# Kernel optimization log

Measured on AMD Instinct MI355X. Metric: run time of the kernel, lower is better.

## Reference

```python
import jax, jax.numpy as jnp
import numpy as np

HEADS, OUT_CH = 8, 32  # GATConv(128, 256//8, heads=8) -> concat width 256
NEG_SLOPE = 0.2


def setup_inputs() -> dict:
    key = jax.random.key(0)
    ks = jax.random.split(key, 12)
    N, E, F_IN = 50000, 500000, 128
    H, C = HEADS, OUT_CH
    HID = H * C            # 256
    x = jax.random.normal(ks[0], (N, F_IN), dtype=jnp.float32)
    edge_index = jax.random.randint(ks[1], (2, E), 0, N, dtype=jnp.int64)
    s = 1.0 / np.sqrt(F_IN)
    W_gat = jax.random.normal(ks[2], (F_IN, H * C), dtype=jnp.float32) * s
    att_src = jax.random.normal(ks[3], (H, C), dtype=jnp.float32) * (1.0 / np.sqrt(C))
    att_dst = jax.random.normal(ks[4], (H, C), dtype=jnp.float32) * (1.0 / np.sqrt(C))
    b_gat = jnp.zeros((HID,), dtype=jnp.float32)
    W1 = jax.random.normal(ks[5], (HID, HID // 2), dtype=jnp.float32) * (1.0 / np.sqrt(HID))
    b1 = jnp.zeros((HID // 2,), dtype=jnp.float32)
    W2 = jax.random.normal(ks[6], (HID // 2, 6), dtype=jnp.float32) * (1.0 / np.sqrt(HID // 2))
    b2 = jnp.zeros((6,), dtype=jnp.float32)
    return {"x": x, "edge_index": edge_index, "W_gat": W_gat, "att_src": att_src,
            "att_dst": att_dst, "b_gat": b_gat, "W1": W1, "b1": b1, "W2": W2, "b2": b2}


def _gat_forward(x, edge_index, W_gat, att_src, att_dst, b_gat):
    N = x.shape[0]
    H, C = HEADS, OUT_CH
    # add self loops (PyG GATConv default)
    loop = jnp.arange(N, dtype=edge_index.dtype)
    src = jnp.concatenate([edge_index[0], loop])
    dst = jnp.concatenate([edge_index[1], loop])
    # per-node transform: [N, H, C]
    xh = (x @ W_gat).reshape(N, H, C)
    a_src = jnp.einsum('nhc,hc->nh', xh, att_src)  # [N, H]
    a_dst = jnp.einsum('nhc,hc->nh', xh, att_dst)  # [N, H]
    alpha = a_src[src] + a_dst[dst]                # [Etot, H]
    alpha = jnp.where(alpha >= 0, alpha, NEG_SLOPE * alpha)  # leaky relu
    # segment softmax over destination nodes
    m = jax.ops.segment_max(alpha, dst, num_segments=N)     # [N, H]
    m = jax.lax.stop_gradient(m)
    ex = jnp.exp(alpha - m[dst])
    denom = jax.ops.segment_sum(ex, dst, num_segments=N)    # [N, H]
    coef = ex / denom[dst]                                   # [Etot, H]
    # weighted scatter-add aggregation
    msgs = xh[src] * coef[:, :, None]                        # [Etot, H, C]
    out = jax.ops.segment_sum(msgs, dst, num_segments=N)     # [N, H, C]
    return out.reshape(N, H * C) + b_gat


def reference(x, edge_index, W_gat, att_src, att_dst, b_gat, W1, b1, W2, b2):
    h = _gat_forward(x, edge_index, W_gat, att_src, att_dst, b_gat)
    h = jax.nn.elu(h)
    g = jnp.mean(h, axis=0, keepdims=True)   # [1, 256] mean pool
    g = jax.nn.relu(g @ W1 + b1)
    return g @ W2 + b2                        # [1, 6] logits
```

## Files before the change

kernel.cpp:

```cpp
#include <hip/hip_runtime.h>
#include <hip/hip_fp8.h>
#include <math.h>

#define F_IN 128
#define HID 256
#define NH 8
#define CAP 40

typedef _Float16 h16;
typedef __attribute__((ext_vector_type(8))) _Float16 half8;
typedef __attribute__((ext_vector_type(4))) float f32x4;

__device__ inline unsigned char f32_to_fp8(float v) {
#if __has_builtin(__builtin_amdgcn_cvt_pk_fp8_f32)
    return (unsigned char)(__builtin_amdgcn_cvt_pk_fp8_f32(v, v, 0, false) & 0xff);
#else
    __hip_fp8_e4m3 t(v);
    return (unsigned char)t.__x;
#endif
}

__device__ inline void fp8x4_to_f32(int w, float* out) {
#if __has_builtin(__builtin_amdgcn_cvt_pk_f32_fp8)
    auto lo = __builtin_amdgcn_cvt_pk_f32_fp8(w, false);
    auto hi = __builtin_amdgcn_cvt_pk_f32_fp8(w, true);
    out[0] = lo[0]; out[1] = lo[1]; out[2] = hi[0]; out[3] = hi[1];
#else
    #pragma unroll
    for (int k = 0; k < 4; ++k) {
        __hip_fp8_e4m3 t;
        t.__x = (unsigned char)((w >> (8 * k)) & 0xff);
        out[k] = (float)t;
    }
#endif
}

__global__ void k_prep(const float* __restrict__ Wg, h16* __restrict__ Wt_sw,
                       int* cnt, float* g2, int n) {
    int i = blockIdx.x * 256 + threadIdx.x;
    if (i < n) cnt[i] = 0;
    if (i < 256 * HID) g2[i] = 0.f;
    if (i < 4096) {
        int fid = i;
        int lane16 = fid & 15;
        int quad = (fid >> 4) & 3;
        int ks = (fid >> 6) & 3;
        int ct = fid >> 8;
        int col = ct * 16 + lane16;
        int k0 = ks * 32 + quad * 8;
        half8 v;
        #pragma unroll
        for (int j = 0; j < 8; ++j) v[j] = (h16)Wg[(size_t)(k0 + j) * HID + col];
        *(half8*)(Wt_sw + (size_t)fid * 8) = v;
    }
}

__global__ __launch_bounds__(512) void k_gemmsc(const float* __restrict__ x,
                                                const h16* __restrict__ Wt_sw,
                                                const float* __restrict__ att_s,
                                                const float* __restrict__ att_d,
                                                const int* __restrict__ srcp,
                                                const int* __restrict__ dstp,
                                                unsigned char* __restrict__ xh8,
                                                float* __restrict__ a_src,
                                                float* __restrict__ a_dst,
                                                int* cnt, unsigned short* __restrict__ bin,
                                                int n, int e, int ntiles) {
    __shared__ h16 wlds[32768];
    int t = threadIdx.x;
    {
        const int4* wsrc = (const int4*)Wt_sw;
        int4* wdst = (int4*)wlds;
        #pragma unroll
        for (int i = 0; i < 8; ++i) wdst[i * 512 + t] = wsrc[i * 512 + t];
    }
    __syncthreads();
    int w = t >> 6, l = t & 63;
    int lane16 = l & 15, quad = l >> 4;
    const h16* wl = wlds + (size_t)l * 8;

    if (w >= 6) {
        for (int i = blockIdx.x * 128 + (w - 6) * 64 + l; i < e; i += gridDim.x * 128) {
            int d = dstp[i];
            int pos = atomicAdd(&cnt[d], 1);
            if (pos < CAP) bin[(size_t)d * CAP + pos] = (unsigned short)srcp[i];
        }
        return;
    }
    for (int tile = blockIdx.x * 6 + w; tile < ntiles; tile += gridDim.x * 6) {
        int row0 = tile * 16;
        int rA = row0 + lane16;
        if (rA >= n) rA = n - 1;
        const float* xrow = x + (size_t)rA * F_IN + quad * 8;
        half8 afr[4];
        #pragma unroll
        for (int ks = 0; ks < 4; ++ks) {
            float4 v0 = *(const float4*)(xrow + ks * 32);
            float4 v1 = *(const float4*)(xrow + ks * 32 + 4);
            half8 a;
            a[0] = (h16)v0.x; a[1] = (h16)v0.y; a[2] = (h16)v0.z; a[3] = (h16)v0.w;
            a[4] = (h16)v1.x; a[5] = (h16)v1.y; a[6] = (h16)v1.z; a[7] = (h16)v1.w;
            afr[ks] = a;
        }
        f32x4 acc[16];
        #pragma unroll
        for (int ct = 0; ct < 16; ++ct) acc[ct] = (f32x4){0.f, 0.f, 0.f, 0.f};
        #pragma unroll
        for (int ct = 0; ct < 16; ++ct) {
            #pragma unroll
            for (int ks = 0; ks < 4; ++ks) {
                half8 b = *(const half8*)(wl + (ct * 4 + ks) * 512);
                acc[ct] = __builtin_amdgcn_mfma_f32_16x16x32_f16(afr[ks], b, acc[ct], 0, 0, 0);
            }
        }
        if (row0 + 16 <= n) {
            #pragma unroll
            for (int ct = 0; ct < 16; ++ct) {
                int col = ct * 16 + lane16;
                #pragma unroll
                for (int r = 0; r < 4; ++r)
                    xh8[(size_t)(row0 + quad * 4 + r) * HID + col] = f32_to_fp8(acc[ct][r]);
            }
        } else {
            #pragma unroll
            for (int ct = 0; ct < 16; ++ct) {
                int col = ct * 16 + lane16;
                #pragma unroll
                for (int r = 0; r < 4; ++r) {
                    int row = row0 + quad * 4 + r;
                    if (row < n) xh8[(size_t)row * HID + col] = f32_to_fp8(acc[ct][r]);
                }
            }
        }
        #pragma unroll
        for (int h = 0; h < 8; ++h) {
            float ps[4] = {0.f, 0.f, 0.f, 0.f};
            float pd[4] = {0.f, 0.f, 0.f, 0.f};
            #pragma unroll
            for (int cc = 0; cc < 2; ++cc) {
                int ct = h * 2 + cc;
                float as_ = att_s[ct * 16 + lane16];
                float ad_ = att_d[ct * 16 + lane16];
                #pragma unroll
                for (int r = 0; r < 4; ++r) {
                    ps[r] += acc[ct][r] * as_;
                    pd[r] += acc[ct][r] * ad_;
                }
            }
            #pragma unroll
            for (int m = 1; m < 16; m <<= 1) {
                #pragma unroll
                for (int r = 0; r < 4; ++r) {
                    ps[r] += __shfl_xor(ps[r], m, 64);
                    pd[r] += __shfl_xor(pd[r], m, 64);
                }
            }
            if (lane16 == 0) {
                #pragma unroll
                for (int r = 0; r < 4; ++r) {
                    int row = row0 + quad * 4 + r;
                    if (row < n) {
                        a_src[row * NH + h] = ps[r];
                        a_dst[row * NH + h] = pd[r];
                    }
                }
            }
        }
    }
}

__global__ __launch_bounds__(256) void k_agg(const unsigned char* __restrict__ xh8,
                                             const float* __restrict__ a_src,
                                             const float* __restrict__ a_dst,
                                             const int* __restrict__ cnt,
                                             const unsigned short* __restrict__ bin,
                                             const float* __restrict__ b_gat,
                                             float* __restrict__ g2, int n) {
    __shared__ float wpart[4][260];
    int t = threadIdx.x;
    int slot = t >> 4;
    int cl = t & 15;
    int c0 = cl * 16;
    int h = cl >> 1;
    int nn = blockIdx.x * 16 + slot;
    bool alive = nn < n;
    int nnc = alive ? nn : (n - 1);

    float ad = a_dst[nnc * NH + h];
    int deg = cnt[nnc];
    if (deg > CAP) deg = CAP;

    float al = a_src[nnc * NH + h] + ad;
    al = al > 0.f ? al : 0.2f * al;
    float ex = __expf(al);
    float den = ex;
    float acc[16];
    {
        int4 v = *(const int4*)(xh8 + (size_t)nnc * HID + c0);
        float f[16];
        fp8x4_to_f32(v.x, f); fp8x4_to_f32(v.y, f + 4);
        fp8x4_to_f32(v.z, f + 8); fp8x4_to_f32(v.w, f + 12);
        #pragma unroll
        for (int i = 0; i < 16; ++i) acc[i] = ex * f[i];
    }
    const unsigned short* brow = bin + (size_t)nnc * CAP;
    int j = 0;
    for (; j + 4 <= deg; j += 4) {
        ushort4 ss = *(const ushort4*)(brow + j);
        int s0 = ss.x, s1 = ss.y, s2 = ss.z, s3 = ss.w;
        float aa[4];
        aa[0] = a_src[s0 * NH + h];
        aa[1] = a_src[s1 * NH + h];
        aa[2] = a_src[s2 * NH + h];
        aa[3] = a_src[s3 * NH + h];
        int4 v0 = *(const int4*)(xh8 + (size_t)s0 * HID + c0);
        int4 v1 = *(const int4*)(xh8 + (size_t)s1 * HID + c0);
        int4 v2 = *(const int4*)(xh8 + (size_t)s2 * HID + c0);
        int4 v3 = *(const int4*)(xh8 + (size_t)s3 * HID + c0);
        float e4[4];
        #pragma unroll
        for (int q = 0; q < 4; ++q) {
            float a2 = aa[q] + ad;
            a2 = a2 > 0.f ? a2 : 0.2f * a2;
            e4[q] = __expf(a2);
            den += e4[q];
        }
        float f[16];
        fp8x4_to_f32(v0.x, f); fp8x4_to_f32(v0.y, f + 4);
        fp8x4_to_f32(v0.z, f + 8); fp8x4_to_f32(v0.w, f + 12);
        #pragma unroll
        for (int i = 0; i < 16; ++i) acc[i] += e4[0] * f[i];
        fp8x4_to_f32(v1.x, f); fp8x4_to_f32(v1.y, f + 4);
        fp8x4_to_f32(v1.z, f + 8); fp8x4_to_f32(v1.w, f + 12);
        #pragma unroll
        for (int i = 0; i < 16; ++i) acc[i] += e4[1] * f[i];
        fp8x4_to_f32(v2.x, f); fp8x4_to_f32(v2.y, f + 4);
        fp8x4_to_f32(v2.z, f + 8); fp8x4_to_f32(v2.w, f + 12);
        #pragma unroll
        for (int i = 0; i < 16; ++i) acc[i] += e4[2] * f[i];
        fp8x4_to_f32(v3.x, f); fp8x4_to_f32(v3.y, f + 4);
        fp8x4_to_f32(v3.z, f + 8); fp8x4_to_f32(v3.w, f + 12);
        #pragma unroll
        for (int i = 0; i < 16; ++i) acc[i] += e4[3] * f[i];
    }
    for (; j < deg; ++j) {
        int s = brow[j];
        float a2 = a_src[s * NH + h] + ad;
        a2 = a2 > 0.f ? a2 : 0.2f * a2;
        float e2 = __expf(a2);
        den += e2;
        int4 v = *(const int4*)(xh8 + (size_t)s * HID + c0);
        float f[16];
        fp8x4_to_f32(v.x, f); fp8x4_to_f32(v.y, f + 4);
        fp8x4_to_f32(v.z, f + 8); fp8x4_to_f32(v.w, f + 12);
        #pragma unroll
        for (int i = 0; i < 16; ++i) acc[i] += e2 * f[i];
    }
    float inv = 1.f / den;
    float val[16];
    #pragma unroll
    for (int q = 0; q < 4; ++q) {
        float4 bv = *(const float4*)(b_gat + c0 + q * 4);
        val[q * 4 + 0] = acc[q * 4 + 0] * inv + bv.x;
        val[q * 4 + 1] = acc[q * 4 + 1] * inv + bv.y;
        val[q * 4 + 2] = acc[q * 4 + 2] * inv + bv.z;
        val[q * 4 + 3] = acc[q * 4 + 3] * inv + bv.w;
    }
    #pragma unroll
    for (int i = 0; i < 16; ++i) {
        float v = val[i];
        v = v > 0.f ? v : expm1f(v);
        val[i] = alive ? v : 0.f;
    }
    #pragma unroll
    for (int i = 0; i < 16; ++i) {
        val[i] += __shfl_xor(val[i], 16, 64);
        val[i] += __shfl_xor(val[i], 32, 64);
    }
    int w = t >> 6, lw = t & 63;
    if (lw < 16) {
        #pragma unroll
        for (int q = 0; q < 4; ++q)
            *(f32x4*)(&wpart[w][c0 + q * 4]) =
                (f32x4){val[q * 4], val[q * 4 + 1], val[q * 4 + 2], val[q * 4 + 3]};
    }
    __syncthreads();
    float s = wpart[0][t] + wpart[1][t] + wpart[2][t] + wpart[3][t];
    atomicAdd(&g2[(blockIdx.x & 255) * HID + t], s);
}

__global__ __launch_bounds__(256) void k_mlp(const float* __restrict__ g2,
                                             const float* __restrict__ W1,
                                             const float* __restrict__ b1,
                                             const float* __restrict__ W2,
                                             const float* __restrict__ b2,
                                             float* __restrict__ out, int n) {
    __shared__ float gm[HID];
    __shared__ float h1p[2][128];
    __shared__ float h1[128];
    int t = threadIdx.x;
    float s = 0.f;
    for (int b = 0; b < 256; ++b) s += g2[b * HID + t];
    gm[t] = s / (float)n;
    __syncthreads();
    int o = t & 127, hf = t >> 7;
    float a = 0.f;
    #pragma unroll 4
    for (int k = hf * 128; k < hf * 128 + 128; ++k) a += gm[k] * W1[k * 128 + o];
    h1p[hf][o] = a;
    __syncthreads();
    if (t < 128) {
        float v = h1p[0][t] + h1p[1][t] + b1[t];
        h1[t] = v > 0.f ? v : 0.f;
    }
    __syncthreads();
    if (t < 6) {
        float a2 = b2[t];
        for (int k = 0; k < 128; ++k) a2 += h1[k] * W2[k * 6 + t];
        out[t] = a2;
    }
}

extern "C" void kernel_launch(void* const* d_in, const int* in_sizes, int n_in,
                              void* d_out, int out_size, void* d_ws, size_t ws_size,
                              hipStream_t stream) {
    const float* x     = (const float*)d_in[0];
    const int*   ei    = (const int*)d_in[1];
    const float* Wg    = (const float*)d_in[2];
    const float* att_s = (const float*)d_in[3];
    const float* att_d = (const float*)d_in[4];
    const float* b_gat = (const float*)d_in[5];
    const float* W1    = (const float*)d_in[6];
    const float* b1    = (const float*)d_in[7];
    const float* W2    = (const float*)d_in[8];
    const float* b2    = (const float*)d_in[9];

    int N = in_sizes[0] / F_IN;
    int E = in_sizes[1] / 2;
    const int* srcp = ei;
    const int* dstp = ei + E;
    int nblk = (N + 15) / 16;
    int ntiles = (N + 15) / 16;

    char* ws = (char*)d_ws;
    size_t off = 0;
    auto alloc = [&](size_t bytes) {
        size_t o = off;
        off += (bytes + 255) & ~(size_t)255;
        return o;
    };
    unsigned char* xh8 = (unsigned char*)(ws + alloc((size_t)N * HID));
    h16*   Wt      = (h16*)(ws + alloc((size_t)F_IN * HID * 2));
    float* asr     = (float*)(ws + alloc((size_t)N * NH * 4));
    float* ads     = (float*)(ws + alloc((size_t)N * NH * 4));
    int*   cnt     = (int*)(ws + alloc((size_t)N * 4));
    unsigned short* bin = (unsigned short*)(ws + alloc((size_t)N * CAP * 2));
    float* g2      = (float*)(ws + alloc((size_t)256 * HID * 4));

    k_prep<<<(N + 255) / 256, 256, 0, stream>>>(Wg, Wt, cnt, g2, N);
    k_gemmsc<<<512, 512, 0, stream>>>(x, Wt, att_s, att_d, srcp, dstp,
                                      xh8, asr, ads, cnt, bin, N, E, ntiles);
    k_agg<<<nblk, 256, 0, stream>>>(xh8, asr, ads, cnt, bin, b_gat, g2, N);
    k_mlp<<<1, 256, 0, stream>>>(g2, W1, b1, W2, b2, (float*)d_out, N);
}
```

Baseline: 176.7 us.

## Replace global atomic binning with two-pass bucketed partition and separate GEMM kernel

Edge binning by destination moves out of the GEMM kernel into two new kernels. The first partitions edges into 256-node buckets using shared-memory histograms and one global atomic per bucket per block. The second builds the per-node CAP-limited lists in LDS and writes them out with coalesced stores. This removes the per-edge global atomics and scattered 2-byte writes. The GEMM kernel now runs one tile per wave and issues its x loads before the weight LDS fill so they overlap, at the cost of two extra launches and a bucket buffer that drops edges past BCAP.

```diff
diff --git a/kernel.cpp b/kernel.cpp
--- a/kernel.cpp
+++ b/kernel.cpp
@@ -6,6 +6,7 @@
 #define HID 256
 #define NH 8
 #define CAP 40
+#define BCAP 4096
 
 typedef _Float16 h16;
 typedef __attribute__((ext_vector_type(8))) _Float16 half8;
@@ -36,9 +37,9 @@
 }
 
 __global__ void k_prep(const float* __restrict__ Wg, h16* __restrict__ Wt_sw,
-                       int* cnt, float* g2, int n) {
+                       int* gcur, float* g2, int n) {
     int i = blockIdx.x * 256 + threadIdx.x;
-    if (i < n) cnt[i] = 0;
+    if (i < 256) gcur[i] = 0;
     if (i < 256 * HID) g2[i] = 0.f;
     if (i < 4096) {
         int fid = i;
@@ -55,19 +56,105 @@
     }
 }
 
-__global__ __launch_bounds__(512) void k_gemmsc(const float* __restrict__ x,
-                                                const h16* __restrict__ Wt_sw,
-                                                const float* __restrict__ att_s,
-                                                const float* __restrict__ att_d,
-                                                const int* __restrict__ srcp,
-                                                const int* __restrict__ dstp,
-                                                unsigned char* __restrict__ xh8,
-                                                float* __restrict__ a_src,
-                                                float* __restrict__ a_dst,
-                                                int* cnt, unsigned short* __restrict__ bin,
-                                                int n, int e, int ntiles) {
+__global__ __launch_bounds__(256) void k_part(const int* __restrict__ dstp,
+                                              const int* __restrict__ srcp,
+                                              unsigned int* __restrict__ gbuck,
+                                              int* __restrict__ gcur,
+                                              int e, int nbuck) {
+    __shared__ int hist[256];
+    __shared__ int base[256];
+    __shared__ int cur[256];
+    int t = threadIdx.x;
+    int c0 = blockIdx.x * 4096;
+    hist[t] = 0;
+    __syncthreads();
+    #pragma unroll
+    for (int j = 0; j < 16; ++j) {
+        int i = c0 + j * 256 + t;
+        if (i < e) atomicAdd(&hist[dstp[i] >> 8], 1);
+    }
+    __syncthreads();
+    if (t < nbuck && hist[t] > 0) base[t] = atomicAdd(&gcur[t], hist[t]);
+    cur[t] = 0;
+    __syncthreads();
+    #pragma unroll
+    for (int j = 0; j < 16; ++j) {
+        int i = c0 + j * 256 + t;
+        if (i < e) {
+            int d = dstp[i];
+            int b = d >> 8;
+            int pos = base[b] + atomicAdd(&cur[b], 1);
+            if (pos < BCAP)
+                gbuck[(size_t)b * BCAP + pos] =
+                    ((unsigned)(d & 255) << 16) | (unsigned)srcp[i];
+        }
+    }
+}
+
+__global__ __launch_bounds__(256) void k_bin(const unsigned int* __restrict__ gbuck,
+                                             const int* __restrict__ gcur,
+                                             int* __restrict__ cnt,
+                                             unsigned short* __restrict__ bin,
+                                             int n, int nbuck) {
+    __shared__ int hist[256];
+    __shared__ int cur[256];
+    __shared__ __align__(16) unsigned short bl[256 * CAP];
+    int t = threadIdx.x;
+    int b = blockIdx.x;
+    int count = gcur[b];
+    if (count > BCAP) count = BCAP;
+    hist[t] = 0;
+    __syncthreads();
+    const unsigned int* bb = gbuck + (size_t)b * BCAP;
+    for (int j = t; j < count; j += 256) atomicAdd(&hist[(bb[j] >> 16) & 255], 1);
+    __syncthreads();
+    int node = b * 256 + t;
+    if (node < n) {
+        int hh = hist[t];
+        cnt[node] = hh > CAP ? CAP : hh;
+    }
+    cur[t] = 0;
+    __syncthreads();
+    for (int j = t; j < count; j += 256) {
+        unsigned int wv = bb[j];
+        int dl = (wv >> 16) & 255;
+        int pos = atomicAdd(&cur[dl], 1);
+        if (pos < CAP) bl[dl * CAP + pos] = (unsigned short)(wv & 0xffff);
+    }
+    __syncthreads();
+    const int4* s4 = (const int4*)bl;
+    int4* d4 = (int4*)(bin + (size_t)b * 256 * CAP);
+    #pragma unroll
+    for (int q = 0; q < 5; ++q) d4[q * 256 + t] = s4[q * 256 + t];
+}
+
+__global__ __launch_bounds__(512) void k_gemm(const float* __restrict__ x,
+                                              const h16* __restrict__ Wt_sw,
+                                              const float* __restrict__ att_s,
+                                              const float* __restrict__ att_d,
+                                              unsigned char* __restrict__ xh8,
+                                              float* __restrict__ a_src,
+                                              float* __restrict__ a_dst,
+                                              int n, int ntiles) {
     __shared__ h16 wlds[32768];
     int t = threadIdx.x;
+    int w = t >> 6, l = t & 63;
+    int lane16 = l & 15, quad = l >> 4;
+
+    float4 pv0[4], pv1[4];
+    int tile = blockIdx.x * 8 + w;
+    bool have = tile < ntiles;
+    int row0 = tile * 16;
+    if (have) {
+        int rA = row0 + lane16;
+        if (rA >= n) rA = n - 1;
+        const float* xrow = x + (size_t)rA * F_IN + quad * 8;
+        #pragma unroll
+        for (int ks = 0; ks < 4; ++ks) {
+            pv0[ks] = *(const float4*)(xrow + ks * 32);
+            pv1[ks] = *(const float4*)(xrow + ks * 32 + 4);
+        }
+    }
     {
         const int4* wsrc = (const int4*)Wt_sw;
         int4* wdst = (int4*)wlds;
@@ -75,94 +162,79 @@
         for (int i = 0; i < 8; ++i) wdst[i * 512 + t] = wsrc[i * 512 + t];
     }
     __syncthreads();
-    int w = t >> 6, l = t & 63;
-    int lane16 = l & 15, quad = l >> 4;
+    if (!have) return;
     const h16* wl = wlds + (size_t)l * 8;
 
-    if (w >= 6) {
-        for (int i = blockIdx.x * 128 + (w - 6) * 64 + l; i < e; i += gridDim.x * 128) {
-            int d = dstp[i];
-            int pos = atomicAdd(&cnt[d], 1);
-            if (pos < CAP) bin[(size_t)d * CAP + pos] = (unsigned short)srcp[i];
-        }
-        return;
-    }
-    for (int tile = blockIdx.x * 6 + w; tile < ntiles; tile += gridDim.x * 6) {
-        int row0 = tile * 16;
-        int rA = row0 + lane16;
-        if (rA >= n) rA = n - 1;
-        const float* xrow = x + (size_t)rA * F_IN + quad * 8;
-        half8 afr[4];
+    half8 afr[4];
+    #pragma unroll
+    for (int ks = 0; ks < 4; ++ks) {
+        half8 a;
+        a[0] = (h16)pv0[ks].x; a[1] = (h16)pv0[ks].y;
+        a[2] = (h16)pv0[ks].z; a[3] = (h16)pv0[ks].w;
+        a[4] = (h16)pv1[ks].x; a[5] = (h16)pv1[ks].y;
+        a[6] = (h16)pv1[ks].z; a[7] = (h16)pv1[ks].w;
+        afr[ks] = a;
+    }
+    f32x4 acc[16];
+    #pragma unroll
+    for (int ct = 0; ct < 16; ++ct) acc[ct] = (f32x4){0.f, 0.f, 0.f, 0.f};
+    #pragma unroll
+    for (int ct = 0; ct < 16; ++ct) {
         #pragma unroll
         for (int ks = 0; ks < 4; ++ks) {
-            float4 v0 = *(const float4*)(xrow + ks * 32);
-            float4 v1 = *(const float4*)(xrow + ks * 32 + 4);
-            half8 a;
-            a[0] = (h16)v0.x; a[1] = (h16)v0.y; a[2] = (h16)v0.z; a[3] = (h16)v0.w;
-            a[4] = (h16)v1.x; a[5] = (h16)v1.y; a[6] = (h16)v1.z; a[7] = (h16)v1.w;
-            afr[ks] = a;
-        }
-        f32x4 acc[16];
-        #pragma unroll
-        for (int ct = 0; ct < 16; ++ct) acc[ct] = (f32x4){0.f, 0.f, 0.f, 0.f};
+            half8 bfr = *(const half8*)(wl + (ct * 4 + ks) * 512);
+            acc[ct] = __builtin_amdgcn_mfma_f32_16x16x32_f16(afr[ks], bfr, acc[ct], 0, 0, 0);
+        }
+    }
+    if (row0 + 16 <= n) {
         #pragma unroll
         for (int ct = 0; ct < 16; ++ct) {
+            int col = ct * 16 + lane16;
             #pragma unroll
-            for (int ks = 0; ks < 4; ++ks) {
-                half8 b = *(const half8*)(wl + (ct * 4 + ks) * 512);
-                acc[ct] = __builtin_amdgcn_mfma_f32_16x16x32_f16(afr[ks], b, acc[ct], 0, 0, 0);
+            for (int r = 0; r < 4; ++r)
+                xh8[(size_t)(row0 + quad * 4 + r) * HID + col] = f32_to_fp8(acc[ct][r]);
+        }
+    } else {
+        #pragma unroll
+        for (int ct = 0; ct < 16; ++ct) {
+            int col = ct * 16 + lane16;
+            #pragma unroll
+            for (int r = 0; r < 4; ++r) {
+                int row = row0 + quad * 4 + r;
+                if (row < n) xh8[(size_t)row * HID + col] = f32_to_fp8(acc[ct][r]);
             }
         }
-        if (row0 + 16 <= n) {
+    }
+    #pragma unroll
+    for (int h = 0; h < 8; ++h) {
+        float ps[4] = {0.f, 0.f, 0.f, 0.f};
+        float pd[4] = {0.f, 0.f, 0.f, 0.f};
+        #pragma unroll
+        for (int cc = 0; cc < 2; ++cc) {
+            int ct = h * 2 + cc;
+            float as_ = att_s[ct * 16 + lane16];
+            float ad_ = att_d[ct * 16 + lane16];
             #pragma unroll
-            for (int ct = 0; ct < 16; ++ct) {
-                int col = ct * 16 + lane16;
-                #pragma unroll
-                for (int r = 0; r < 4; ++r)
-                    xh8[(size_t)(row0 + quad * 4 + r) * HID + col] = f32_to_fp8(acc[ct][r]);
+            for (int r = 0; r < 4; ++r) {
+                ps[r] += acc[ct][r] * as_;
+                pd[r] += acc[ct][r] * ad_;
             }
-        } else {
+        }
+        #pragma unroll
+        for (int m = 1; m < 16; m <<= 1) {
             #pragma unroll
-            for (int ct = 0; ct < 16; ++ct) {
-                int col = ct * 16 + lane16;
-                #pragma unroll
-                for (int r = 0; r < 4; ++r) {
-                    int row = row0 + quad * 4 + r;
-                    if (row < n) xh8[(size_t)row * HID + col] = f32_to_fp8(acc[ct][r]);
-                }
+            for (int r = 0; r < 4; ++r) {
+                ps[r] += __shfl_xor(ps[r], m, 64);
+                pd[r] += __shfl_xor(pd[r], m, 64);
             }
         }
-        #pragma unroll
-        for (int h = 0; h < 8; ++h) {
-            float ps[4] = {0.f, 0.f, 0.f, 0.f};
-            float pd[4] = {0.f, 0.f, 0.f, 0.f};
+        if (lane16 == 0) {
             #pragma unroll
-            for (int cc = 0; cc < 2; ++cc) {
-                int ct = h * 2 + cc;
-                float as_ = att_s[ct * 16 + lane16];
-                float ad_ = att_d[ct * 16 + lane16];
-                #pragma unroll
-                for (int r = 0; r < 4; ++r) {
-                    ps[r] += acc[ct][r] * as_;
-                    pd[r] += acc[ct][r] * ad_;
-                }
-            }
-            #pragma unroll
-            for (int m = 1; m < 16; m <<= 1) {
-                #pragma unroll
-                for (int r = 0; r < 4; ++r) {
-                    ps[r] += __shfl_xor(ps[r], m, 64);
-                    pd[r] += __shfl_xor(pd[r], m, 64);
-                }
-            }
-            if (lane16 == 0) {
-                #pragma unroll
-                for (int r = 0; r < 4; ++r) {
-                    int row = row0 + quad * 4 + r;
-                    if (row < n) {
-                        a_src[row * NH + h] = ps[r];
-                        a_dst[row * NH + h] = pd[r];
-                    }
+            for (int r = 0; r < 4; ++r) {
+                int row = row0 + quad * 4 + r;
+                if (row < n) {
+                    a_src[row * NH + h] = ps[r];
+                    a_dst[row * NH + h] = pd[r];
                 }
             }
         }
@@ -341,6 +413,7 @@
     const int* dstp = ei + E;
     int nblk = (N + 15) / 16;
     int ntiles = (N + 15) / 16;
+    int nbuck = (N + 255) >> 8;
 
     char* ws = (char*)d_ws;
     size_t off = 0;
@@ -354,12 +427,18 @@
     float* asr     = (float*)(ws + alloc((size_t)N * NH * 4));
     float* ads     = (float*)(ws + alloc((size_t)N * NH * 4));
     int*   cnt     = (int*)(ws + alloc((size_t)N * 4));
-    unsigned short* bin = (unsigned short*)(ws + alloc((size_t)N * CAP * 2));
+    unsigned short* bin = (unsigned short*)(ws + alloc((size_t)nbuck * 256 * CAP * 2));
     float* g2      = (float*)(ws + alloc((size_t)256 * HID * 4));
-
-    k_prep<<<(N + 255) / 256, 256, 0, stream>>>(Wg, Wt, cnt, g2, N);
-    k_gemmsc<<<512, 512, 0, stream>>>(x, Wt, att_s, att_d, srcp, dstp,
-                                      xh8, asr, ads, cnt, bin, N, E, ntiles);
+    unsigned int* gbuck = (unsigned int*)(ws + alloc((size_t)nbuck * BCAP * 4));
+    int*   gcur    = (int*)(ws + alloc((size_t)256 * 4));
+
+    int nb1 = (E + 4095) / 4096;
+    int ngemm = (ntiles + 7) / 8;
+
+    k_prep<<<256, 256, 0, stream>>>(Wg, Wt, gcur, g2, N);
+    k_part<<<nb1, 256, 0, stream>>>(dstp, srcp, gbuck, gcur, E, nbuck);
+    k_bin<<<nbuck, 256, 0, stream>>>(gbuck, gcur, cnt, bin, N, nbuck);
+    k_gemm<<<ngemm, 512, 0, stream>>>(x, Wt, att_s, att_d, xh8, asr, ads, N, ntiles);
     k_agg<<<nblk, 256, 0, stream>>>(xh8, asr, ads, cnt, bin, b_gat, g2, N);
     k_mlp<<<1, 256, 0, stream>>>(g2, W1, b1, W2, b2, (float*)d_out, N);
 }
```

New measurement: 188.7 us. 1.07x slower.
